# Optimization experiments

Hardware: AMD Instinct MI355X
Metric: run time of the kernel (lower is better)

Reference implementation:

```python
import jax, jax.numpy as jnp
import numpy as np

B, T, E, H, D = 2, 1024, 2048, 16, 64
DEPTH = 12
LAMBDA_INIT = 0.8 - 0.6 * float(np.exp(-0.3 * DEPTH))
EPS = 1e-5


def _rope_interleaved(x):
    # x: (b, t, heads, d), rotate interleaved even/odd pairs
    d = x.shape[-1]
    inv_freq = 1.0 / (10000.0 ** (jnp.arange(0, d, 2, dtype=jnp.float32) / d))  # (d/2,)
    ang = jnp.arange(x.shape[1], dtype=jnp.float32)[:, None] * inv_freq[None, :]  # (t, d/2)
    cos = jnp.cos(ang)[None, :, None, :].astype(x.dtype)
    sin = jnp.sin(ang)[None, :, None, :].astype(x.dtype)
    x1, x2 = x[..., 0::2], x[..., 1::2]
    r1 = x1 * cos - x2 * sin
    r2 = x1 * sin + x2 * cos
    return jnp.stack([r1, r2], axis=-1).reshape(x.shape)


def setup_inputs() -> dict:
    key = jax.random.key(0)
    ks = jax.random.split(key, 11)
    w_scale = 0.02
    return {
        "x": jax.random.normal(ks[0], (B, T, E), jnp.float32),
        "rel_pos": jax.random.uniform(ks[1], (T, D), jnp.float32),
        "wq": jax.random.normal(ks[2], (E, E), jnp.float32) * w_scale,
        "wk": jax.random.normal(ks[3], (E, E), jnp.float32) * w_scale,
        "wv": jax.random.normal(ks[4], (E, E), jnp.float32) * w_scale,
        "lambda_q1": jax.random.normal(ks[5], (D,), jnp.float32) * 0.1,
        "lambda_q2": jax.random.normal(ks[6], (D,), jnp.float32) * 0.1,
        "lambda_k1": jax.random.normal(ks[7], (D,), jnp.float32) * 0.1,
        "lambda_k2": jax.random.normal(ks[8], (D,), jnp.float32) * 0.1,
        "subln_w": jnp.ones((2 * D,), jnp.float32),
        "wo": jax.random.normal(ks[9], (E, E), jnp.float32) * w_scale,
    }


def reference(x, rel_pos, wq, wk, wv, lambda_q1, lambda_q2, lambda_k1, lambda_k2, subln_w, wo):
    b, t, e = x.shape
    scaling = D ** 0.5
    # projections; q,k have 2*H heads of dim D, v has H heads of dim 2*D
    q = (x @ wq.T).reshape(b, t, 2 * H, D)
    k = (x @ wk.T).reshape(b, t, 2 * H, D)
    v = (x @ wv.T).reshape(b, t, H, 2 * D)
    k = k * rel_pos[None, :, None, :]
    q = _rope_interleaved(q)
    k = _rope_interleaved(k)
    q = q.transpose(0, 2, 1, 3)  # (b, 2H, t, D)
    k = k.transpose(0, 2, 1, 3)
    v = v.transpose(0, 2, 1, 3)  # (b, H, t, 2D)
    scores = jnp.einsum("bhqd,bhkd->bhqk", q, k) / scaling
    causal = jnp.tril(jnp.ones((t, t), bool))
    scores = jnp.where(causal[None, None], scores, jnp.float32(-1e9))
    p = jax.nn.softmax(scores.astype(jnp.float32), axis=-1).astype(x.dtype)
    lam1 = jnp.exp(jnp.sum(lambda_q1 * lambda_k1))
    lam2 = jnp.exp(jnp.sum(lambda_q2 * lambda_k2))
    lam_full = lam1 - lam2 + LAMBDA_INIT
    p = p.reshape(b, H, 2, t, t)
    pw = p[:, :, 0] - lam_full * p[:, :, 1]  # (b, H, t, t)
    attn = jnp.einsum("bhqk,bhkd->bhqd", pw, v)  # (b, H, t, 2D)
    # RMSNorm over last dim (2D)
    ms = jnp.mean(attn.astype(jnp.float32) ** 2, axis=-1, keepdims=True)
    attn = (attn * jax.lax.rsqrt(ms + EPS)).astype(x.dtype) * subln_w
    out = attn.transpose(0, 2, 1, 3).reshape(b, t, H * 2 * D) @ wo.T
    return out
```

## Files before the change

### kernel.cpp

```cpp
#include <hip/hip_runtime.h>

typedef __bf16 bf16x8 __attribute__((ext_vector_type(8)));
typedef float f32x4 __attribute__((ext_vector_type(4)));

__device__ __forceinline__ float bf2f(unsigned short u) {
  return __uint_as_float(((unsigned)u) << 16);
}
__device__ __forceinline__ unsigned short f2bf(float f) {
  unsigned u = __float_as_uint(f);
  return (unsigned short)((u + 0x7fffu + ((u >> 16) & 1u)) >> 16);
}
__device__ __forceinline__ unsigned pack2(float a, float b) {
  return (unsigned)f2bf(a) | ((unsigned)f2bf(b) << 16);
}

#define SWZB(row, byte) ((byte) ^ (((row) & 7) << 4))

#define AS_GLOBAL(p) ((const __attribute__((address_space(1))) void*)(p))
#define AS_LDS(p) ((__attribute__((address_space(3))) void*)(p))

__global__ __launch_bounds__(256) void pre_kernel(
    const float* __restrict__ s0, const float* __restrict__ s1,
    const float* __restrict__ s2, const float* __restrict__ s3,
    unsigned short* __restrict__ d0, unsigned short* __restrict__ d1,
    unsigned short* __restrict__ d2, unsigned short* __restrict__ d3,
    const float* __restrict__ lq1, const float* __restrict__ lq2,
    const float* __restrict__ lk1, const float* __restrict__ lk2,
    float* __restrict__ lamb, int n4) {
  if (blockIdx.y == 4) {
    if (blockIdx.x == 0 && threadIdx.x < 64) {
      int l = threadIdx.x;
      float p1 = lq1[l] * lk1[l];
      float p2 = lq2[l] * lk2[l];
      #pragma unroll
      for (int off = 32; off; off >>= 1) {
        p1 += __shfl_xor(p1, off);
        p2 += __shfl_xor(p2, off);
      }
      if (l == 0) lamb[0] = expf(p1) - expf(p2) + 0.7836057665316245f;
    }
    return;
  }
  int idx = blockIdx.x * 256 + threadIdx.x;
  if (idx >= n4) return;
  const float* s;
  unsigned short* d;
  switch (blockIdx.y) {
    case 0: s = s0; d = d0; break;
    case 1: s = s1; d = d1; break;
    case 2: s = s2; d = d2; break;
    default: s = s3; d = d3; break;
  }
  float4 v = reinterpret_cast<const float4*>(s)[idx];
  uint2 pk;
  pk.x = pack2(v.x, v.y);
  pk.y = pack2(v.z, v.w);
  reinterpret_cast<uint2*>(d)[idx] = pk;
}

template <typename OT>
__global__ __launch_bounds__(256)
void gemm_bk64(const unsigned short* __restrict__ A, const unsigned short* __restrict__ Bw,
               OT* __restrict__ C, int M, int K, int ldc) {
  __shared__ __align__(16) unsigned short As[128 * 64];
  __shared__ __align__(16) unsigned short Bs[128 * 64];
  const int tid = threadIdx.x;
  const int bm = blockIdx.x * 128, bn = blockIdx.y * 128;
  const int lane = tid & 63, wave = tid >> 6;
  const int wm = (wave >> 1) * 64, wn = (wave & 1) * 64;
  const int rr = lane & 15, lg = lane >> 4;
  const int srow = lane >> 3;
  const int sblk = (lane & 7) ^ srow;
  const char* ab = reinterpret_cast<const char*>(As);
  const char* bb = reinterpret_cast<const char*>(Bs);
  OT* Cb = C + (size_t)(bn / ldc) * ((size_t)M * ldc) + (bn % ldc);
  f32x4 acc[4][4] = {};
  for (int kt = 0; kt < K; kt += 64) {
    __syncthreads();
    #pragma unroll
    for (int j = 0; j < 4; ++j) {
      int s = wave + j * 4;
      const unsigned short* asrc = &A[(long)(bm + s * 8 + srow) * K + kt + sblk * 8];
      __builtin_amdgcn_global_load_lds(AS_GLOBAL(asrc), AS_LDS(&As[s * 512]), 16, 0, 0);
      const unsigned short* bsrc = &Bw[(long)(bn + s * 8 + srow) * K + kt + sblk * 8];
      __builtin_amdgcn_global_load_lds(AS_GLOBAL(bsrc), AS_LDS(&Bs[s * 512]), 16, 0, 0);
    }
    __syncthreads();
    bf16x8 af[4][2], bq[4][2];
    #pragma unroll
    for (int i = 0; i < 4; ++i) {
      int row = wm + i * 16 + rr;
      af[i][0] = *reinterpret_cast<const bf16x8*>(ab + row * 128 + SWZB(row, lg * 16));
      af[i][1] = *reinterpret_cast<const bf16x8*>(ab + row * 128 + SWZB(row, 64 + lg * 16));
    }
    #pragma unroll
    for (int j = 0; j < 4; ++j) {
      int row = wn + j * 16 + rr;
      bq[j][0] = *reinterpret_cast<const bf16x8*>(bb + row * 128 + SWZB(row, lg * 16));
      bq[j][1] = *reinterpret_cast<const bf16x8*>(bb + row * 128 + SWZB(row, 64 + lg * 16));
    }
    #pragma unroll
    for (int i = 0; i < 4; ++i)
      #pragma unroll
      for (int j = 0; j < 4; ++j) {
        acc[i][j] = __builtin_amdgcn_mfma_f32_16x16x32_bf16(af[i][0], bq[j][0], acc[i][j], 0, 0, 0);
        acc[i][j] = __builtin_amdgcn_mfma_f32_16x16x32_bf16(af[i][1], bq[j][1], acc[i][j], 0, 0, 0);
      }
  }
  const int cc = lane & 15;
  #pragma unroll
  for (int i = 0; i < 4; ++i)
    #pragma unroll
    for (int j = 0; j < 4; ++j)
      #pragma unroll
      for (int r = 0; r < 4; ++r) {
        long row = bm + wm + i * 16 + lg * 4 + r;
        long col = wn + j * 16 + cc;
        float v = acc[i][j][r];
        if constexpr (sizeof(OT) == 2) Cb[row * ldc + col] = f2bf(v);
        else                           Cb[row * ldc + col] = v;
      }
}

#define ROPE_BLKS 8192
#define CVT_BLKS 4096
#define TRN_BLKS 1024
__global__ __launch_bounds__(256) void mid_kernel(
    const unsigned short* __restrict__ qraw, const unsigned short* __restrict__ kraw,
    const unsigned short* __restrict__ vraw, const float* __restrict__ rel,
    const float* __restrict__ wo,
    unsigned short* __restrict__ qatt, unsigned short* __restrict__ katt,
    unsigned short* __restrict__ wob, unsigned short* __restrict__ vtb) {
  __shared__ unsigned short ls[64][68];
  const int bid = blockIdx.x;
  const int tid = threadIdx.x;
  if (bid < 2 * ROPE_BLKS) {
    const int use_rel = bid >= ROPE_BLKS;
    const unsigned short* raw = use_rel ? kraw : qraw;
    unsigned short* outp = use_rel ? katt : qatt;
    int idx = (bid & (ROPE_BLKS - 1)) * 256 + tid;
    int i = idx & 31;
    int t = (idx >> 5) & 1023;
    int hp = (idx >> 15) & 31;
    int b = idx >> 20;
    int src = (b * 1024 + t) * 2048 + hp * 64 + 2 * i;
    unsigned pair = *reinterpret_cast<const unsigned*>(&raw[src]);
    float x1 = __uint_as_float(pair << 16);
    float x2 = __uint_as_float(pair & 0xffff0000u);
    if (use_rel) {
      x1 *= rel[t * 64 + 2 * i];
      x2 *= rel[t * 64 + 2 * i + 1];
    }
    float inv = expf(-0.28782313662425574f * (float)i);
    float s, c;
    sincosf((float)t * inv, &s, &c);
    int dst = ((b * 32 + hp) * 1024 + t) * 64 + 2 * i;
    *reinterpret_cast<unsigned*>(&outp[dst]) = pack2(x1 * c - x2 * s, x1 * s + x2 * c);
  } else if (bid < 2 * ROPE_BLKS + CVT_BLKS) {
    int idx = (bid - 2 * ROPE_BLKS) * 256 + tid;
    float4 v = reinterpret_cast<const float4*>(wo)[idx];
    uint2 pk;
    pk.x = pack2(v.x, v.y);
    pk.y = pack2(v.z, v.w);
    reinterpret_cast<uint2*>(wob)[idx] = pk;
  } else {
    int tb = bid - (2 * ROPE_BLKS + CVT_BLKS);
    const int t0 = (tb & 15) * 64, n0 = ((tb >> 4) & 31) * 64, b = tb >> 9;
    #pragma unroll
    for (int p = 0; p < 4; ++p) {
      int idx = p * 256 + tid;
      int tl = idx >> 4, nq = (idx & 15) * 4;
      *reinterpret_cast<uint2*>(&ls[tl][nq]) = *reinterpret_cast<const uint2*>(
          &vraw[((long)(b * 1024 + t0 + tl)) * 2048 + n0 + nq]);
    }
    __syncthreads();
    #pragma unroll
    for (int p = 0; p < 4; ++p) {
      int idx = p * 256 + tid;
      int nl = idx >> 4, tq = (idx & 15) * 4;
      uint2 o;
      o.x = (unsigned)ls[tq + 0][nl] | ((unsigned)ls[tq + 1][nl] << 16);
      o.y = (unsigned)ls[tq + 2][nl] | ((unsigned)ls[tq + 3][nl] << 16);
      *reinterpret_cast<uint2*>(&vtb[((long)(b * 2048 + n0 + nl)) * 1024 + t0 + tq]) = o;
    }
  }
}

__global__ __launch_bounds__(256) void attn_mfma(
    const unsigned short* __restrict__ Qa,
    const unsigned short* __restrict__ Ka,
    const unsigned short* __restrict__ Vt,
    const float* __restrict__ lam_p,
    const float* __restrict__ subln,
    unsigned short* __restrict__ O) {
  const int n = blockIdx.x;
  const int c = n & 7, m = n >> 3;
  const int g = c * 4 + (m >> 4);
  const int bx = m & 15;
  const int h = g & 15, b = g >> 4;

  const int tid = threadIdx.x;
  const int lane = tid & 63, w = tid >> 6;
  const int lg = lane >> 4, cc = lane & 15;
  const int hh = w >> 1, qoff = (w & 1) * 16;

  __shared__ __align__(16) unsigned short KsBuf[2 * 64 * 64];
  __shared__ __align__(16) unsigned short VsBuf[128 * 64];
  __shared__ __align__(16) unsigned short PbBuf[4 * 16 * 64];

  const float lam = lam_p[0];
  char* ksb = reinterpret_cast<char*>(&KsBuf[0]);
  char* vsb = reinterpret_cast<char*>(&VsBuf[0]);
  char* pbb = reinterpret_cast<char*>(PbBuf) + w * 2048;
  float* cb = reinterpret_cast<float*>(&KsBuf[0]);

  const int srow = lane >> 3;
  const int sblk = (lane & 7) ^ srow;
  auto STAGE = [&](int k0) {
    #pragma unroll
    for (int j = 0; j < 4; ++j) {
      int s = w * 4 + j;
      int sh = s >> 3, rg = s & 7;
      const unsigned short* ksrc =
          &Ka[(((long)(b * 32 + 2 * h + sh)) * 1024 + k0 + rg * 8 + srow) * 64 + sblk * 8];
      __builtin_amdgcn_global_load_lds(AS_GLOBAL(ksrc), AS_LDS(ksb + sh * 8192 + rg * 1024),
                                       16, 0, 0);
      const unsigned short* vsrc =
          &Vt[((long)(b * 2048 + h * 128 + s * 8 + srow)) * 1024 + k0 + sblk * 8];
      __builtin_amdgcn_global_load_lds(AS_GLOBAL(vsrc), AS_LDS(vsb + s * 1024), 16, 0, 0);
    }
  };

  float sl[8];
  #pragma unroll
  for (int jc = 0; jc < 8; ++jc) sl[jc] = subln[jc * 16 + cc];

  const long kbase = (long)((b * 32 + 2 * h + hh) * 1024);

  for (int pass = 0; pass < 2; ++pass) {
    const int q0 = (pass ? (31 - bx) : bx) * 32;
    const int nt = ((q0 + 31) >> 6) + 1;

    bf16x8 qf[2];
    {
      const long qrow = q0 + qoff + cc;
      #pragma unroll
      for (int c2 = 0; c2 < 2; ++c2)
        qf[c2] = *reinterpret_cast<const bf16x8*>(&Qa[(kbase + qrow) * 64 + c2 * 32 + lg * 8]);
    }
    f32x4 acc_o[8];
    float mS[4], lS[4];
    #pragma unroll
    for (int jc = 0; jc < 8; ++jc) acc_o[jc] = (f32x4){0.f, 0.f, 0.f, 0.f};
    #pragma unroll
    for (int r = 0; r < 4; ++r) { mS[r] = -1e30f; lS[r] = 0.f; }

    for (int tile = 0; tile < nt; ++tile) {
      const int k0 = tile * 64;
      __syncthreads();
      STAGE(k0);
      __syncthreads();

      f32x4 s4[4];
      #pragma unroll
      for (int j = 0; j < 4; ++j) s4[j] = (f32x4){0.f, 0.f, 0.f, 0.f};
      #pragma unroll
      for (int j = 0; j < 4; ++j) {
        int row = j * 16 + cc;
        const char* base = ksb + hh * 8192 + row * 128;
        bf16x8 kb0 = *reinterpret_cast<const bf16x8*>(base + SWZB(row, lg * 16));
        bf16x8 kb1 = *reinterpret_cast<const bf16x8*>(base + SWZB(row, lg * 16 + 64));
        s4[j] = __builtin_amdgcn_mfma_f32_16x16x32_bf16(qf[0], kb0, s4[j], 0, 0, 0);
        s4[j] = __builtin_amdgcn_mfma_f32_16x16x32_bf16(qf[1], kb1, s4[j], 0, 0, 0);
      }
      #pragma unroll
      for (int j = 0; j < 4; ++j) {
        int kcol = k0 + j * 16 + cc;
        #pragma unroll
        for (int r = 0; r < 4; ++r) {
          int qrow = q0 + qoff + lg * 4 + r;
          float s = s4[j][r] * 0.125f;
          s4[j][r] = (kcol > qrow) ? -1e30f : s;
        }
      }
      float rescv[4];
      #pragma unroll
      for (int r = 0; r < 4; ++r) {
        float mx = fmaxf(fmaxf(s4[0][r], s4[1][r]), fmaxf(s4[2][r], s4[3][r]));
        mx = fmaxf(mx, __shfl_xor(mx, 1));
        mx = fmaxf(mx, __shfl_xor(mx, 2));
        mx = fmaxf(mx, __shfl_xor(mx, 4));
        mx = fmaxf(mx, __shfl_xor(mx, 8));
        float mold = mS[r];
        float mnew = fmaxf(mold, mx);
        mS[r] = mnew;
        float rsc = __expf(mold - mnew);
        rescv[r] = rsc;
        float ls = 0.f;
        #pragma unroll
        for (int j = 0; j < 4; ++j) {
          float p = __expf(s4[j][r] - mnew);
          s4[j][r] = p;
          ls += p;
        }
        ls += __shfl_xor(ls, 1);
        ls += __shfl_xor(ls, 2);
        ls += __shfl_xor(ls, 4);
        ls += __shfl_xor(ls, 8);
        lS[r] = lS[r] * rsc + ls;
      }
      #pragma unroll
      for (int j = 0; j < 4; ++j)
        #pragma unroll
        for (int r = 0; r < 4; ++r) {
          int rowl = lg * 4 + r;
          *reinterpret_cast<unsigned short*>(
              pbb + rowl * 128 + SWZB(rowl, (j * 16 + cc) * 2)) = f2bf(s4[j][r]);
        }

      bf16x8 pa[2];
      #pragma unroll
      for (int c2 = 0; c2 < 2; ++c2)
        pa[c2] = *reinterpret_cast<const bf16x8*>(pbb + cc * 128 + SWZB(cc, lg * 16 + c2 * 64));
      #pragma unroll
      for (int jc = 0; jc < 8; ++jc)
        #pragma unroll
        for (int r = 0; r < 4; ++r)
          acc_o[jc][r] *= rescv[r];
      #pragma unroll
      for (int jc = 0; jc < 8; ++jc) {
        int row = jc * 16 + cc;
        const char* base = vsb + row * 128;
        bf16x8 vf0 = *reinterpret_cast<const bf16x8*>(base + SWZB(row, lg * 16));
        bf16x8 vf1 = *reinterpret_cast<const bf16x8*>(base + SWZB(row, lg * 16 + 64));
        acc_o[jc] = __builtin_amdgcn_mfma_f32_16x16x32_bf16(pa[0], vf0, acc_o[jc], 0, 0, 0);
        acc_o[jc] = __builtin_amdgcn_mfma_f32_16x16x32_bf16(pa[1], vf1, acc_o[jc], 0, 0, 0);
      }
    }

    __syncthreads();
    if (hh == 1) {
      #pragma unroll
      for (int r = 0; r < 4; ++r) {
        float inv2 = lam / lS[r];
        int row = qoff + lg * 4 + r;
        #pragma unroll
        for (int jc = 0; jc < 8; ++jc)
          cb[row * 128 + ((jc ^ (row & 7)) * 16 + cc)] = acc_o[jc][r] * inv2;
      }
    }
    __syncthreads();
    if (hh == 0) {
      float sc[4];
      #pragma unroll
      for (int r = 0; r < 4; ++r) {
        float inv1 = 1.f / lS[r];
        int row = qoff + lg * 4 + r;
        float ss = 0.f;
        #pragma unroll
        for (int jc = 0; jc < 8; ++jc) {
          float at = acc_o[jc][r] * inv1 - cb[row * 128 + ((jc ^ (row & 7)) * 16 + cc)];
          acc_o[jc][r] = at;
          ss += at * at;
        }
        ss += __shfl_xor(ss, 1);
        ss += __shfl_xor(ss, 2);
        ss += __shfl_xor(ss, 4);
        ss += __shfl_xor(ss, 8);
        sc[r] = rsqrtf(ss * (1.f / 128.f) + 1e-5f);
      }
      #pragma unroll
      for (int r = 0; r < 4; ++r) {
        long qrow = q0 + qoff + lg * 4 + r;
        #pragma unroll
        for (int jc = 0; jc < 8; ++jc) {
          O[(long)(b * 1024 + qrow) * 2048 + h * 128 + jc * 16 + cc] =
              f2bf(acc_o[jc][r] * sc[r] * sl[jc]);
        }
      }
    }
    __syncthreads();
  }
}

extern "C" void kernel_launch(void* const* d_in, const int* in_sizes, int n_in,
                              void* d_out, int out_size, void* d_ws, size_t ws_size,
                              hipStream_t stream) {
  (void)in_sizes; (void)n_in; (void)out_size; (void)ws_size;
  const float* x    = (const float*)d_in[0];
  const float* rel  = (const float*)d_in[1];
  const float* wq   = (const float*)d_in[2];
  const float* wk   = (const float*)d_in[3];
  const float* wv   = (const float*)d_in[4];
  const float* lq1  = (const float*)d_in[5];
  const float* lq2  = (const float*)d_in[6];
  const float* lk1  = (const float*)d_in[7];
  const float* lk2  = (const float*)d_in[8];
  const float* subw = (const float*)d_in[9];
  const float* wo   = (const float*)d_in[10];
  float* out = (float*)d_out;

  char* ws = (char*)d_ws;
  const size_t SZ = (size_t)2048 * 2048 * 2;
  unsigned short* wqkvb = (unsigned short*)(ws);
  unsigned short* vtb   = (unsigned short*)(ws);
  unsigned short* qatt  = (unsigned short*)(ws + SZ);
  unsigned short* katt  = (unsigned short*)(ws + 2 * SZ);
  unsigned short* xbf   = (unsigned short*)(ws + 3 * SZ);
  unsigned short* wob   = xbf;
  unsigned short* qraw  = (unsigned short*)(ws + 4 * SZ);
  unsigned short* kraw  = (unsigned short*)(ws + 5 * SZ);
  unsigned short* vraw  = (unsigned short*)(ws + 6 * SZ);
  unsigned short* aout  = qraw;
  float* lamb           = (float*)(ws + 7 * SZ);

  const int N4 = 2048 * 2048 / 4;
  pre_kernel<<<dim3(N4 / 256, 5), 256, 0, stream>>>(
      x, wq, wk, wv, xbf, wqkvb, wqkvb + (size_t)2048 * 2048,
      wqkvb + (size_t)2 * 2048 * 2048, lq1, lq2, lk1, lk2, lamb, N4);

  gemm_bk64<unsigned short><<<dim3(16, 48), 256, 0, stream>>>(xbf, wqkvb, qraw,
                                                              2048, 2048, 2048);

  mid_kernel<<<2 * ROPE_BLKS + CVT_BLKS + TRN_BLKS, 256, 0, stream>>>(
      qraw, kraw, vraw, rel, wo, qatt, katt, wob, vtb);

  attn_mfma<<<dim3(512), 256, 0, stream>>>(qatt, katt, vtb, lamb, subw, aout);

  gemm_bk64<float><<<dim3(16, 16), 256, 0, stream>>>(aout, wob, out, 2048, 2048, 2048);
}
```

Baseline: 193.0 us.

## Load K/V fragments directly from global memory instead of staging through LDS

The attention kernel no longer stages K and V tiles into shared memory with global_load_lds and block barriers. Each wave now reads its K and V MFMA operands straight from global memory (relying on L1/L2), and the RMSNorm combine buffer gets its own LDS allocation. This removes two barriers per tile and the LDS round trip, but the two waves that share a head now each fetch the same V data, and the global loads are narrower and less coalesced.

```diff
diff --git a/kernel.cpp b/kernel.cpp
--- a/kernel.cpp
+++ b/kernel.cpp
@@ -204,38 +204,20 @@
   const int lg = lane >> 4, cc = lane & 15;
   const int hh = w >> 1, qoff = (w & 1) * 16;
 
-  __shared__ __align__(16) unsigned short KsBuf[2 * 64 * 64];
-  __shared__ __align__(16) unsigned short VsBuf[128 * 64];
   __shared__ __align__(16) unsigned short PbBuf[4 * 16 * 64];
+  __shared__ __align__(16) float CbBuf[32 * 128];
 
   const float lam = lam_p[0];
-  char* ksb = reinterpret_cast<char*>(&KsBuf[0]);
-  char* vsb = reinterpret_cast<char*>(&VsBuf[0]);
   char* pbb = reinterpret_cast<char*>(PbBuf) + w * 2048;
-  float* cb = reinterpret_cast<float*>(&KsBuf[0]);
-
-  const int srow = lane >> 3;
-  const int sblk = (lane & 7) ^ srow;
-  auto STAGE = [&](int k0) {
-    #pragma unroll
-    for (int j = 0; j < 4; ++j) {
-      int s = w * 4 + j;
-      int sh = s >> 3, rg = s & 7;
-      const unsigned short* ksrc =
-          &Ka[(((long)(b * 32 + 2 * h + sh)) * 1024 + k0 + rg * 8 + srow) * 64 + sblk * 8];
-      __builtin_amdgcn_global_load_lds(AS_GLOBAL(ksrc), AS_LDS(ksb + sh * 8192 + rg * 1024),
-                                       16, 0, 0);
-      const unsigned short* vsrc =
-          &Vt[((long)(b * 2048 + h * 128 + s * 8 + srow)) * 1024 + k0 + sblk * 8];
-      __builtin_amdgcn_global_load_lds(AS_GLOBAL(vsrc), AS_LDS(vsb + s * 1024), 16, 0, 0);
-    }
-  };
+  float* cb = CbBuf;
 
   float sl[8];
   #pragma unroll
   for (int jc = 0; jc < 8; ++jc) sl[jc] = subln[jc * 16 + cc];
 
   const long kbase = (long)((b * 32 + 2 * h + hh) * 1024);
+  const unsigned short* Kg = &Ka[kbase * 64];
+  const unsigned short* Vg = &Vt[((long)(b * 2048 + h * 128)) * 1024];
 
   for (int pass = 0; pass < 2; ++pass) {
     const int q0 = (pass ? (31 - bx) : bx) * 32;
@@ -257,19 +239,16 @@
 
     for (int tile = 0; tile < nt; ++tile) {
       const int k0 = tile * 64;
-      __syncthreads();
-      STAGE(k0);
-      __syncthreads();
 
       f32x4 s4[4];
       #pragma unroll
       for (int j = 0; j < 4; ++j) s4[j] = (f32x4){0.f, 0.f, 0.f, 0.f};
       #pragma unroll
       for (int j = 0; j < 4; ++j) {
-        int row = j * 16 + cc;
-        const char* base = ksb + hh * 8192 + row * 128;
-        bf16x8 kb0 = *reinterpret_cast<const bf16x8*>(base + SWZB(row, lg * 16));
-        bf16x8 kb1 = *reinterpret_cast<const bf16x8*>(base + SWZB(row, lg * 16 + 64));
+        int row = k0 + j * 16 + cc;
+        const unsigned short* kr = &Kg[(long)row * 64 + lg * 8];
+        bf16x8 kb0 = *reinterpret_cast<const bf16x8*>(kr);
+        bf16x8 kb1 = *reinterpret_cast<const bf16x8*>(kr + 32);
         s4[j] = __builtin_amdgcn_mfma_f32_16x16x32_bf16(qf[0], kb0, s4[j], 0, 0, 0);
         s4[j] = __builtin_amdgcn_mfma_f32_16x16x32_bf16(qf[1], kb1, s4[j], 0, 0, 0);
       }
@@ -330,9 +309,9 @@
       #pragma unroll
       for (int jc = 0; jc < 8; ++jc) {
         int row = jc * 16 + cc;
-        const char* base = vsb + row * 128;
-        bf16x8 vf0 = *reinterpret_cast<const bf16x8*>(base + SWZB(row, lg * 16));
-        bf16x8 vf1 = *reinterpret_cast<const bf16x8*>(base + SWZB(row, lg * 16 + 64));
+        const unsigned short* vr = &Vg[(long)row * 1024 + k0 + lg * 8];
+        bf16x8 vf0 = *reinterpret_cast<const bf16x8*>(vr);
+        bf16x8 vf1 = *reinterpret_cast<const bf16x8*>(vr + 32);
         acc_o[jc] = __builtin_amdgcn_mfma_f32_16x16x32_bf16(pa[0], vf0, acc_o[jc], 0, 0, 0);
         acc_o[jc] = __builtin_amdgcn_mfma_f32_16x16x32_bf16(pa[1], vf1, acc_o[jc], 0, 0, 0);
       }
@@ -379,7 +358,6 @@
         }
       }
     }
-    __syncthreads();
   }
 }
 
```

Result: slower. 241.2 us (+25.0%).
